# Optimization experiments

Hardware: AMD Instinct MI355X
Metric: run time of the kernel (lower is better)

The kernel has to match this reference:

```python
import jax, jax.numpy as jnp
import numpy as np

B = 4096        # number of (drug, disease) pair graphs
N_PER = 60      # nodes per subgraph (>= k)
N = B * N_PER   # 245760 total nodes
E = 2_000_000   # edges
F_IN = 64
L1, L2 = 32, 32 # latent_dim
K = 30          # sort-pool k
N_DRUG, N_DIS = 1024, 2048


def gcn_conv(x, src, dst, W, b, n):
    # PyG GCNConv (eval): h = XW; symmetric norm with self-loops; out = A_hat h + b
    h = x @ W
    deg = jax.ops.segment_sum(jnp.ones(src.shape[0], h.dtype), dst, num_segments=n) + 1.0
    dinv = deg ** -0.5
    msg = h[src] * (dinv[src] * dinv[dst])[:, None]
    out = jax.ops.segment_sum(msg, dst, num_segments=n)
    out = out + h * (dinv * dinv)[:, None]  # self-loop contribution
    return out + b


def dense_gcn(x, adj, W, b):
    # PyG DenseGCNConv: set diag to 1, D^-1/2 A D^-1/2, out = A_hat (x W) + b
    n = adj.shape[0]
    eye = jnp.eye(n, dtype=adj.dtype)
    a = adj * (1.0 - eye) + eye
    deg = a.sum(-1)
    dinv = jnp.where(deg > 0, deg ** -0.5, 0.0)
    a = dinv[:, None] * a * dinv[None, :]
    return a @ (x @ W) + b


def conv1d(x, w, b, stride):
    out = jax.lax.conv_general_dilated(x, w, (stride,), 'VALID',
                                       dimension_numbers=('NCH', 'OIH', 'NCH'))
    return out + b[None, :, None]


def setup_inputs():
    key = jax.random.key(0)
    ks = jax.random.split(key, 24)
    x = jax.random.normal(ks[0], (N, F_IN), jnp.float32)
    edge_index = jax.random.randint(ks[1], (2, E), 0, N)
    batch = jnp.repeat(jnp.arange(B), N_PER)
    node = jnp.stack([jax.random.randint(ks[2], (B,), 0, N_DRUG),
                      jax.random.randint(ks[3], (B,), 0, N_DIS)], axis=1)
    di_sim = jax.random.normal(ks[4], (N_DRUG, N_DRUG), jnp.float32)
    dr_sim = jax.random.normal(ks[5], (N_DIS, N_DIS), jnp.float32)
    drug_adj = jax.random.uniform(ks[6], (N_DRUG, N_DRUG), jnp.float32)
    dis_adj = jax.random.uniform(ks[7], (N_DIS, N_DIS), jnp.float32)
    p = jnp.array(0.5, jnp.float32)

    def w(k, shape):
        return jax.random.normal(k, shape, jnp.float32) * 0.05

    z = lambda s: jnp.zeros(s, jnp.float32)
    params = dict(
        W1=w(ks[8], (F_IN, L1)), b1=z((L1,)),
        W2=w(ks[9], (L1, L2)), b2=z((L2,)),
        W3=w(ks[10], (256, 64)), b3=z((64,)),
        W4=w(ks[11], (64, 16)), b4=z((16,)),
        lin_di_w=w(ks[12], (N_DRUG, 256)), lin_di_b=z((256,)),
        lin_dr_w=w(ks[13], (N_DIS, 256)), lin_dr_b=z((256,)),
        c1_w=w(ks[14], (128, 1, L1 + L2)), c1_b=z((128,)),
        c2_w=w(ks[15], (256, 128, 5)), c2_b=z((256,)),
        lin1_w=w(ks[16], (2816, 128)), lin1_b=z((128,)),
        lin2_w=w(ks[17], (128, 32)), lin2_b=z((32,)),
        bn_g=jnp.ones((32,), jnp.float32), bn_b=z((32,)),
        fcs_w=w(ks[18], (64, 32)), fcs_b=z((32,)),
        fcs2_w=w(ks[19], (32, 1)), fcs2_b=z((1,)),
    )
    return dict(x=x, edge_index=edge_index, batch=batch, node=node,
                di_sim=di_sim, dr_sim=dr_sim, drug_adj=drug_adj,
                dis_adj=dis_adj, p=p, **params)


def reference(x, edge_index, batch, node, di_sim, dr_sim, drug_adj, dis_adj, p,
              W1, b1, W2, b2, W3, b3, W4, b4,
              lin_di_w, lin_di_b, lin_dr_w, lin_dr_b,
              c1_w, c1_b, c2_w, c2_b, lin1_w, lin1_b, lin2_w, lin2_b,
              bn_g, bn_b, fcs_w, fcs_b, fcs2_w, fcs2_b):
    src, dst = edge_index[0], edge_index[1]
    # two GCN layers over the pair subgraphs
    x1 = jax.nn.relu(gcn_conv(x, src, dst, W1, b1, N))
    x2 = jax.nn.relu(gcn_conv(x1, src, dst, W2, b2, N))
    cs = jnp.concatenate([x1, x2], axis=1)       # [N, 64]
    D = cs.shape[1]
    # sort-pool: equal-size graphs, batch contiguous -> reshape and sort per graph
    xb = cs.reshape(B, N_PER, D)
    order = jnp.argsort(-xb[:, :, -1], axis=-1)  # descending by last channel
    xs = jnp.take_along_axis(xb, order[:, :, None], axis=1)[:, :K]  # [B, K, D]
    h = xs.reshape(B, 1, K * D)
    h = jax.nn.relu(conv1d(h, c1_w, c1_b, D))    # [B, 128, K]
    h = jax.lax.reduce_window(h, -jnp.inf, jax.lax.max, (1, 1, 2), (1, 1, 2), 'VALID')
    h = jax.nn.relu(conv1d(h, c2_w, c2_b, 1))    # [B, 256, 11]
    h = h.reshape(B, -1)                         # [B, 2816]
    h = jax.nn.relu(h @ lin1_w + lin1_b)
    h = h @ lin2_w + lin2_b
    h = jax.nn.relu(h * bn_g + bn_b)             # BatchNorm eval (mean 0, var 1)
    # dense similarity-graph branches (conv3/conv4 weights shared across branches)
    di_e = di_sim @ lin_di_w + lin_di_b
    di_f = jax.nn.relu(dense_gcn(di_e, drug_adj, W3, b3))
    di_o = jax.nn.relu(dense_gcn(di_f, drug_adj, W4, b4))
    di = di_o[node[:, 0]]
    dr_e = dr_sim @ lin_dr_w + lin_dr_b
    dr_f = jax.nn.relu(dense_gcn(dr_e, dis_adj, W3, b3))
    dr_o = jax.nn.relu(dense_gcn(dr_f, dis_adj, W4, b4))
    dr = dr_o[node[:, 1]]
    feat = jnp.concatenate([di, dr], axis=1)     # [B, 32]
    z = jnp.concatenate([h * p, feat * (1.0 - p)], axis=1)  # [B, 64]
    z = jax.nn.relu(z @ fcs_w + fcs_b)
    return (z @ fcs2_w + fcs2_b)[:, 0]
```

## Files before the change

kernel.cpp:

```cpp
#include <hip/hip_runtime.h>

#define NN 245760
#define NB 4096
#define NPER 60
#define NE 2000000
#define KSEL 30
#define NDRUG 1024
#define NDIS 2048
#define NBKT 480
#define CHUNK 8192
#define SEGCAP 4992

typedef unsigned short ushort_t;
typedef unsigned int uint_t;
using bf16x8 = __attribute__((ext_vector_type(8))) short;
using f32x4 = __attribute__((ext_vector_type(4))) float;

__device__ inline ushort_t f2bf(float f) {
    union { float f; unsigned int u; } v; v.f = f;
    unsigned int r = v.u + 0x7FFF + ((v.u >> 16) & 1);
    return (ushort_t)(r >> 16);
}

__global__ void k_bcount(const int* __restrict__ ei, int* __restrict__ bcnt) {
    __shared__ int h[NBKT];
    int t = threadIdx.x;
    for (int i = t; i < NBKT; i += 256) h[i] = 0;
    __syncthreads();
    for (int e = blockIdx.x * 256 + t; e < NE; e += gridDim.x * 256)
        atomicAdd(&h[ei[NE + e] >> 9], 1);
    __syncthreads();
    for (int i = t; i < NBKT; i += 256) if (h[i]) atomicAdd(&bcnt[i], h[i]);
}

__global__ void k_bscan(const int* __restrict__ bcnt, int* __restrict__ bofs) {
    __shared__ int a[512], b_[512];
    int t = threadIdx.x;
    int v = (t < NBKT) ? bcnt[t] : 0;
    a[t] = v; __syncthreads();
    int* src = a; int* dst = b_;
    for (int off = 1; off < 512; off <<= 1) {
        dst[t] = src[t] + ((t >= off) ? src[t - off] : 0);
        __syncthreads();
        int* tmp = src; src = dst; dst = tmp;
    }
    if (t < NBKT) bofs[t] = src[t] - v;
}

__global__ __launch_bounds__(256) void k_bscatter(const int* __restrict__ ei,
                                                  const int* __restrict__ bofs,
                                                  int* __restrict__ bfill,
                                                  uint_t* __restrict__ pairs) {
    __shared__ int hist[NBKT], fill[NBKT], gbase[NBKT];
    int t = threadIdx.x;
    long e0 = (long)blockIdx.x * CHUNK;
    int cnt = (int)min((long)CHUNK, (long)NE - e0);
    for (int i = t; i < NBKT; i += 256) { hist[i] = 0; fill[i] = 0; }
    __syncthreads();
    for (int i = t; i < cnt; i += 256)
        atomicAdd(&hist[ei[NE + e0 + i] >> 9], 1);
    __syncthreads();
    for (int i = t; i < NBKT; i += 256)
        if (hist[i]) gbase[i] = bofs[i] + atomicAdd(&bfill[i], hist[i]);
    __syncthreads();
    for (int i = t; i < cnt; i += 256) {
        int s = ei[e0 + i], d = ei[NE + e0 + i];
        int b = d >> 9;
        int pos = gbase[b] + atomicAdd(&fill[b], 1);
        pairs[pos] = ((uint_t)s << 9) | (uint_t)(d & 511);
    }
}

__global__ __launch_bounds__(256) void k_bbuild(const uint_t* __restrict__ pairs,
                                                const int* __restrict__ bofs,
                                                const int* __restrict__ bcnt,
                                                int* __restrict__ csr,
                                                int* __restrict__ rowp,
                                                int* __restrict__ cntg,
                                                float* __restrict__ dinv) {
    __shared__ int hist[512], nbase[512], nfill[512], scanA[512], scanB[512];
    __shared__ int seg[SEGCAP];
    int t = threadIdx.x, b = blockIdx.x;
    int ebase = bofs[b], ecnt = bcnt[b];
    if (ecnt > SEGCAP) ecnt = SEGCAP;
    for (int i = t; i < 512; i += 256) { hist[i] = 0; nfill[i] = 0; }
    __syncthreads();
    for (int i = t; i < ecnt; i += 256)
        atomicAdd(&hist[pairs[ebase + i] & 511], 1);
    __syncthreads();
    for (int i = t; i < 512; i += 256) scanA[i] = hist[i];
    __syncthreads();
    int* src = scanA; int* dst = scanB;
    for (int off = 1; off < 512; off <<= 1) {
        for (int i = t; i < 512; i += 256)
            dst[i] = src[i] + ((i >= off) ? src[i - off] : 0);
        __syncthreads();
        int* tmp = src; src = dst; dst = tmp;
    }
    for (int i = t; i < 512; i += 256) {
        int h = hist[i];
        int excl = src[i] - h;
        nbase[i] = excl;
        int n = (b << 9) + i;
        rowp[n] = ebase + excl;
        cntg[n] = h;
        dinv[n] = 1.0f / sqrtf((float)h + 1.0f);
    }
    __syncthreads();
    for (int i = t; i < ecnt; i += 256) {
        uint_t v = pairs[ebase + i];
        int ln = v & 511;
        int pos = nbase[ln] + atomicAdd(&nfill[ln], 1);
        if (pos < SEGCAP) seg[pos] = (int)(v >> 9);
    }
    __syncthreads();
    for (int i = t; i < ecnt; i += 256) csr[ebase + i] = seg[i];
}

__global__ __launch_bounds__(256) void k_xw(const float* __restrict__ A, const float* __restrict__ W,
                                            float* __restrict__ h, int K, int lda) {
    __shared__ float Xs[64][65];
    __shared__ float Ws[64][32];
    int t = threadIdx.x;
    int r0 = blockIdx.x * 64;
    int kq = K >> 2;
    for (int idx = t; idx < 64 * kq; idx += 256) {
        int row = idx / kq, q = idx % kq;
        float4 v = *(const float4*)(A + (long)(r0 + row) * lda + q * 4);
        Xs[row][q * 4 + 0] = v.x; Xs[row][q * 4 + 1] = v.y;
        Xs[row][q * 4 + 2] = v.z; Xs[row][q * 4 + 3] = v.w;
    }
    for (int idx = t; idx < K * 32; idx += 256) ((float*)Ws)[idx] = W[idx];
    __syncthreads();
    int r = (t >> 3) * 2, c = (t & 7) * 4;
    float4 acc0 = {0, 0, 0, 0}, acc1 = {0, 0, 0, 0};
    for (int k = 0; k < K; k++) {
        float x0 = Xs[r][k], x1 = Xs[r + 1][k];
        float4 w = *(const float4*)&Ws[k][c];
        acc0.x += x0 * w.x; acc0.y += x0 * w.y; acc0.z += x0 * w.z; acc0.w += x0 * w.w;
        acc1.x += x1 * w.x; acc1.y += x1 * w.y; acc1.z += x1 * w.z; acc1.w += x1 * w.w;
    }
    *(float4*)(h + (long)(r0 + r) * 32 + c) = acc0;
    *(float4*)(h + (long)(r0 + r + 1) * 32 + c) = acc1;
}

__global__ void k_gcn_agg(const float* __restrict__ h, const int* __restrict__ csr,
                          const int* __restrict__ rowp, const int* __restrict__ cnt,
                          const float* __restrict__ dinv, const float* __restrict__ bias,
                          float* __restrict__ out, int colofs) {
    int t = threadIdx.x;
    int l = t & 7, g = t >> 3;
    int d = blockIdx.x * 32 + g;
    float dd = dinv[d];
    int start = rowp[d], c = cnt[d];
    float4 hv = *(const float4*)(h + (long)d * 32 + l * 4);
    float4 acc; acc.x = dd * hv.x; acc.y = dd * hv.y; acc.z = dd * hv.z; acc.w = dd * hv.w;
    for (int k = 0; k < c; k++) {
        int s = csr[start + k];
        float ds = dinv[s];
        float4 v = *(const float4*)(h + (long)s * 32 + l * 4);
        acc.x += ds * v.x; acc.y += ds * v.y; acc.z += ds * v.z; acc.w += ds * v.w;
    }
    float4 bv = *(const float4*)(bias + l * 4);
    float* op = out + (long)d * 64 + colofs + l * 4;
    op[0] = fmaxf(dd * acc.x + bv.x, 0.f);
    op[1] = fmaxf(dd * acc.y + bv.y, 0.f);
    op[2] = fmaxf(dd * acc.z + bv.z, 0.f);
    op[3] = fmaxf(dd * acc.w + bv.w, 0.f);
}

__global__ __launch_bounds__(256, 2) void k_conv1_mfma(const float* __restrict__ cs,
                                                       const int* __restrict__ sel,
                                                       const ushort_t* __restrict__ c1w16,
                                                       const float* __restrict__ c1b,
                                                       ushort_t* __restrict__ po16) {
    __shared__ ushort_t A_lds[128 * 72];
    __shared__ ushort_t B_lds[128 * 72];
    int t = threadIdx.x;
    int r0 = blockIdx.x * 128;
#pragma unroll
    for (int rnd = 0; rnd < 4; rnd++) {
        int idx = t + rnd * 256;
        int row = idx >> 3, seg = idx & 7;
        const float* src = cs + (long)sel[r0 + row] * 64 + seg * 8;
        float4 v0 = *(const float4*)src;
        float4 v1 = *(const float4*)(src + 4);
        ushort_t tmp[8] = {f2bf(v0.x), f2bf(v0.y), f2bf(v0.z), f2bf(v0.w),
                           f2bf(v1.x), f2bf(v1.y), f2bf(v1.z), f2bf(v1.w)};
        *(uint4*)&A_lds[row * 72 + seg * 8] = *(uint4*)tmp;
        *(uint4*)&B_lds[row * 72 + seg * 8] = *(const uint4*)(c1w16 + row * 64 + seg * 8);
    }
    __syncthreads();
    int wv = t >> 6, lane = t & 63;
    int wm = wv >> 1, wn = wv & 1;
    int lrow = lane & 15, lk = (lane >> 4) * 8, lr4 = (lane >> 4) * 4;
    f32x4 acc[4][4] = {};
#pragma unroll
    for (int kk = 0; kk < 2; kk++) {
        bf16x8 a[4], b[4];
#pragma unroll
        for (int f = 0; f < 4; f++) {
            a[f] = *(const bf16x8*)&A_lds[(wm * 64 + f * 16 + lrow) * 72 + kk * 32 + lk];
            b[f] = *(const bf16x8*)&B_lds[(wn * 64 + f * 16 + lrow) * 72 + kk * 32 + lk];
        }
#pragma unroll
        for (int i = 0; i < 4; i++)
#pragma unroll
            for (int j = 0; j < 4; j++)
                acc[i][j] = __builtin_amdgcn_mfma_f32_16x16x32_bf16(a[i], b[j], acc[i][j], 0, 0, 0);
    }
    __syncthreads();
    ushort_t* po_lds = A_lds;
#pragma unroll
    for (int fn = 0; fn < 4; fn++) {
        int col = wn * 64 + fn * 16 + lrow;
        float bb = c1b[col];
#pragma unroll
        for (int fm = 0; fm < 4; fm++) {
            int lrow2 = wm * 32 + fm * 8 + (lr4 >> 1);
            float v0 = fmaxf(acc[fm][fn][0] + bb, 0.f);
            float v1 = fmaxf(acc[fm][fn][1] + bb, 0.f);
            float v2 = fmaxf(acc[fm][fn][2] + bb, 0.f);
            float v3 = fmaxf(acc[fm][fn][3] + bb, 0.f);
            po_lds[lrow2 * 128 + col]       = f2bf(fmaxf(v0, v1));
            po_lds[(lrow2 + 1) * 128 + col] = f2bf(fmaxf(v2, v3));
        }
    }
    __syncthreads();
    uint4* dst = (uint4*)(po16 + (long)(r0 >> 1) * 128);
    const uint4* srcp = (const uint4*)po_lds;
#pragma unroll
    for (int i = 0; i < 4; i++) dst[t + i * 256] = srcp[t + i * 256];
}

__global__ __launch_bounds__(256, 2) void k_conv2_mfma(const ushort_t* __restrict__ pool16,
                                                       const ushort_t* __restrict__ w2colT,
                                                       ushort_t* __restrict__ act2,
                                                       const float* __restrict__ bias) {
    __shared__ ushort_t smem[2 * 128 * 72];
    ushort_t* A_lds = smem;
    ushort_t* B_lds = smem + 128 * 72;
    int t = threadIdx.x;
    int r0 = blockIdx.x * 128, c0 = blockIdx.y * 128;
    long abase[4]; const ushort_t* bptr[4]; int lofs[4];
#pragma unroll
    for (int rnd = 0; rnd < 4; rnd++) {
        int idx = t + rnd * 256;
        int row = idx >> 3, seg = idx & 7;
        int arow = r0 + row;
        int bb = arow / 11, tt2 = arow - bb * 11;
        abase[rnd] = (long)(bb * 15 + tt2) * 128 + seg * 8;
        bptr[rnd] = w2colT + (long)(c0 + row) * 640 + seg * 8;
        lofs[rnd] = row * 72 + seg * 8;
    }
    int wv = t >> 6, lane = t & 63;
    int wm = wv >> 1, wn = wv & 1;
    int lrow = lane & 15, lk = (lane >> 4) * 8, lr4 = (lane >> 4) * 4;
    f32x4 acc[4][4] = {};
    for (int k0 = 0; k0 < 640; k0 += 64) {
#pragma unroll
        for (int rnd = 0; rnd < 4; rnd++) {
            *(uint4*)&A_lds[lofs[rnd]] = *(const uint4*)(pool16 + abase[rnd] + k0);
            *(uint4*)&B_lds[lofs[rnd]] = *(const uint4*)(bptr[rnd] + k0);
        }
        __syncthreads();
#pragma unroll
        for (int kk = 0; kk < 2; kk++) {
            bf16x8 a[4], b[4];
#pragma unroll
            for (int f = 0; f < 4; f++) {
                a[f] = *(const bf16x8*)&A_lds[(wm * 64 + f * 16 + lrow) * 72 + kk * 32 + lk];
                b[f] = *(const bf16x8*)&B_lds[(wn * 64 + f * 16 + lrow) * 72 + kk * 32 + lk];
            }
#pragma unroll
            for (int i = 0; i < 4; i++)
#pragma unroll
                for (int j = 0; j < 4; j++)
                    acc[i][j] = __builtin_amdgcn_mfma_f32_16x16x32_bf16(a[i], b[j], acc[i][j], 0, 0, 0);
        }
        __syncthreads();
    }
    ushort_t* c_lds = smem;
#pragma unroll
    for (int fn = 0; fn < 4; fn++) {
        int col = wn * 64 + fn * 16 + lrow;
        float bv = bias[c0 + col];
#pragma unroll
        for (int fm = 0; fm < 4; fm++) {
            int lr = wm * 64 + fm * 16 + lr4;
#pragma unroll
            for (int j = 0; j < 4; j++)
                c_lds[(lr + j) * 128 + col] = f2bf(fmaxf(acc[fm][fn][j] + bv, 0.f));
        }
    }
    __syncthreads();
#pragma unroll
    for (int i = 0; i < 8; i++) {
        int idx = t + i * 256;
        int row = idx >> 4, q = idx & 15;
        *(uint4*)(act2 + (long)(r0 + row) * 256 + c0 + q * 8) = ((const uint4*)c_lds)[idx];
    }
}

__global__ __launch_bounds__(256, 2) void k_lin1_mfma(const ushort_t* __restrict__ A,
                                                      const ushort_t* __restrict__ Bm,
                                                      float* __restrict__ C) {
    __shared__ ushort_t A_lds[128 * 72];
    __shared__ ushort_t B_lds[128 * 72];
    int t = threadIdx.x;
    int r0 = blockIdx.x * 128;
    int kz = blockIdx.z;
    const ushort_t* ap[4]; const ushort_t* bp[4]; int lofs[4];
#pragma unroll
    for (int rnd = 0; rnd < 4; rnd++) {
        int idx = t + rnd * 256;
        int row = idx >> 3, seg = idx & 7;
        ap[rnd] = A + (long)(r0 + row) * 2816 + kz * 704 + seg * 8;
        bp[rnd] = Bm + (long)row * 2816 + kz * 704 + seg * 8;
        lofs[rnd] = row * 72 + seg * 8;
    }
    int wv = t >> 6, lane = t & 63;
    int wm = wv >> 1, wn = wv & 1;
    int lrow = lane & 15, lk = (lane >> 4) * 8, lr4 = (lane >> 4) * 4;
    f32x4 acc[4][4] = {};
    for (int k0 = 0; k0 < 704; k0 += 64) {
#pragma unroll
        for (int rnd = 0; rnd < 4; rnd++) {
            *(uint4*)&A_lds[lofs[rnd]] = *(const uint4*)(ap[rnd] + k0);
            *(uint4*)&B_lds[lofs[rnd]] = *(const uint4*)(bp[rnd] + k0);
        }
        __syncthreads();
#pragma unroll
        for (int kk = 0; kk < 2; kk++) {
            bf16x8 a[4], b[4];
#pragma unroll
            for (int f = 0; f < 4; f++) {
                a[f] = *(const bf16x8*)&A_lds[(wm * 64 + f * 16 + lrow) * 72 + kk * 32 + lk];
                b[f] = *(const bf16x8*)&B_lds[(wn * 64 + f * 16 + lrow) * 72 + kk * 32 + lk];
            }
#pragma unroll
            for (int i = 0; i < 4; i++)
#pragma unroll
                for (int j = 0; j < 4; j++)
                    acc[i][j] = __builtin_amdgcn_mfma_f32_16x16x32_bf16(a[i], b[j], acc[i][j], 0, 0, 0);
        }
        __syncthreads();
    }
#pragma unroll
    for (int fn = 0; fn < 4; fn++) {
        int col = wn * 64 + fn * 16 + lrow;
#pragma unroll
        for (int fm = 0; fm < 4; fm++) {
            int rowb = r0 + wm * 64 + fm * 16 + lr4;
#pragma unroll
            for (int j = 0; j < 4; j++)
                atomicAdd(&C[(long)(rowb + j) * 128 + col], acc[fm][fn][j]);
        }
    }
}

__global__ __launch_bounds__(256, 2) void k_de_mfma(
    const ushort_t* __restrict__ A0, const ushort_t* __restrict__ B0, float* __restrict__ C0,
    const float* __restrict__ bias0, int M0, int K0, int KS0,
    const ushort_t* __restrict__ A1, const ushort_t* __restrict__ B1, float* __restrict__ C1,
    const float* __restrict__ bias1, int M1, int K1, int KS1) {
    __shared__ ushort_t A_lds[128 * 72];
    __shared__ ushort_t B_lds[64 * 72];
    int z = blockIdx.z;
    const ushort_t* A; const ushort_t* Bm; float* C; const float* bias; int M, K, kz, KS;
    if (z < KS0) { A = A0; Bm = B0; C = C0; bias = bias0; M = M0; K = K0; kz = z; KS = KS0; }
    else { A = A1; Bm = B1; C = C1; bias = bias1; M = M1; K = K1; kz = z - KS0; KS = KS1; }
    int r0 = blockIdx.x * 128, c0 = blockIdx.y * 64;
    if (r0 >= M) return;
    int Kc = K / KS;
    int kb = kz * Kc;
    int t = threadIdx.x;
    const ushort_t* ap[4]; int alofs[4];
#pragma unroll
    for (int rnd = 0; rnd < 4; rnd++) {
        int idx = t + rnd * 256;
        int row = idx >> 3, seg = idx & 7;
        ap[rnd] = A + (long)(r0 + row) * K + kb + seg * 8;
        alofs[rnd] = row * 72 + seg * 8;
    }
    const ushort_t* bp[2]; int blofs[2];
#pragma unroll
    for (int rnd = 0; rnd < 2; rnd++) {
        int idx = t + rnd * 256;
        int row = idx >> 3, seg = idx & 7;
        bp[rnd] = Bm + (long)(c0 + row) * K + kb + seg * 8;
        blofs[rnd] = row * 72 + seg * 8;
    }
    int wv = t >> 6, lane = t & 63;
    int lrow = lane & 15, lk = (lane >> 4) * 8, lr4 = (lane >> 4) * 4;
    uint4 areg[4], breg[2];
#pragma unroll
    for (int rnd = 0; rnd < 4; rnd++) areg[rnd] = *(const uint4*)(ap[rnd]);
#pragma unroll
    for (int rnd = 0; rnd < 2; rnd++) breg[rnd] = *(const uint4*)(bp[rnd]);
    f32x4 acc[2][4] = {};
    for (int k0 = 0; k0 < Kc; k0 += 64) {
#pragma unroll
        for (int rnd = 0; rnd < 4; rnd++) *(uint4*)&A_lds[alofs[rnd]] = areg[rnd];
#pragma unroll
        for (int rnd = 0; rnd < 2; rnd++) *(uint4*)&B_lds[blofs[rnd]] = breg[rnd];
        __syncthreads();
        if (k0 + 64 < Kc) {
#pragma unroll
            for (int rnd = 0; rnd < 4; rnd++) areg[rnd] = *(const uint4*)(ap[rnd] + k0 + 64);
#pragma unroll
            for (int rnd = 0; rnd < 2; rnd++) breg[rnd] = *(const uint4*)(bp[rnd] + k0 + 64);
        }
#pragma unroll
        for (int kk = 0; kk < 2; kk++) {
            bf16x8 a[2], b[4];
#pragma unroll
            for (int f = 0; f < 2; f++)
                a[f] = *(const bf16x8*)&A_lds[(wv * 32 + f * 16 + lrow) * 72 + kk * 32 + lk];
#pragma unroll
            for (int f = 0; f < 4; f++)
                b[f] = *(const bf16x8*)&B_lds[(f * 16 + lrow) * 72 + kk * 32 + lk];
#pragma unroll
            for (int i = 0; i < 2; i++)
#pragma unroll
                for (int j = 0; j < 4; j++)
                    acc[i][j] = __builtin_amdgcn_mfma_f32_16x16x32_bf16(a[i], b[j], acc[i][j], 0, 0, 0);
        }
        __syncthreads();
    }
#pragma unroll
    for (int fn = 0; fn < 4; fn++) {
        int col = c0 + fn * 16 + lrow;
        float bv = (kz == 0) ? bias[col] : 0.f;
#pragma unroll
        for (int fm = 0; fm < 2; fm++) {
            int rowb = r0 + wv * 32 + fm * 16 + lr4;
#pragma unroll
            for (int j = 0; j < 4; j++)
                atomicAdd(&C[(long)(rowb + j) * 256 + col], acc[fm][fn][j] + bv);
        }
    }
}

__global__ void k_cvt2(const float* __restrict__ a0, ushort_t* __restrict__ o0, long n0,
                       const float* __restrict__ a1, ushort_t* __restrict__ o1, long n1) {
    long i4 = ((long)blockIdx.x * 256 + threadIdx.x) * 4;
    const float* a; ushort_t* o;
    if (i4 < n0) { a = a0 + i4; o = o0 + i4; }
    else {
        long j = i4 - n0;
        if (j >= n1) return;
        a = a1 + j; o = o1 + j;
    }
    float4 v = *(const float4*)a;
    o[0] = f2bf(v.x); o[1] = f2bf(v.y); o[2] = f2bf(v.z); o[3] = f2bf(v.w);
}

__global__ void k_linwT2(const float* __restrict__ w0, ushort_t* __restrict__ o0, int K0,
                         const float* __restrict__ w1, ushort_t* __restrict__ o1, int K1) {
    __shared__ float tile[64][65];
    int nb0 = K0 / 64;
    int bx = blockIdx.x;
    const float* w; ushort_t* o; int K, kt;
    if (bx < nb0) { w = w0; o = o0; K = K0; kt = bx; }
    else { w = w1; o = o1; K = K1; kt = bx - nb0; }
    int n0 = blockIdx.y * 64, k0 = kt * 64;
    int t = threadIdx.x;
    int r = t >> 6, c = t & 63;
    for (int rr = r; rr < 64; rr += 4)
        tile[rr][c] = w[(long)(k0 + rr) * 256 + n0 + c];
    __syncthreads();
    for (int rr = r; rr < 64; rr += 4)
        o[(long)(n0 + rr) * K + k0 + c] = f2bf(tile[c][rr]);
}

__global__ __launch_bounds__(256) void k_gemm_sk(
    const float* A0, const float* B0, float* C0, const float* ab0p, const float* cs0p,
    int M0, int N0, int K0, int lda0, int KS0, int Kc0,
    const float* A1, const float* B1, float* C1, const float* ab1p, const float* cs1p,
    int M1, int N1, int K1, int lda1, int KS1, int Kc1) {
    int z = blockIdx.z;
    const float* A; const float* Bm; float* C; const float* abp; const float* csp;
    int M, N, K, lda, kz, Kc;
    if (z < KS0) { A = A0; Bm = B0; C = C0; abp = ab0p; csp = cs0p; M = M0; N = N0; K = K0; lda = lda0; kz = z; Kc = Kc0; }
    else { A = A1; Bm = B1; C = C1; abp = ab1p; csp = cs1p; M = M1; N = N1; K = K1; lda = lda1; kz = z - KS0; Kc = Kc1; }
    int r0 = blockIdx.x * 64, c0 = blockIdx.y * 64;
    if (r0 >= M || c0 >= N) return;
    int kb = kz * Kc, ke = min(K, kb + Kc);
    __shared__ float As[16][68];
    __shared__ float Bs[16][68];
    int t = threadIdx.x;
    int tx = t & 15, ty = t >> 4;
    float acc[4][4] = {};
    int ar = t >> 2, aq = (t & 3) * 4;
    long abase = (long)(r0 + ar) * lda;
    int brow = t >> 4, bc = (t & 15) * 4;
    for (int k0 = kb; k0 < ke; k0 += 16) {
        float4 av = *(const float4*)(A + abase + k0 + aq);
        if (abp) {
            float4 abv = *(const float4*)(abp + k0 + aq);
            av.x += abv.x; av.y += abv.y; av.z += abv.z; av.w += abv.w;
        }
        As[aq + 0][ar] = av.x; As[aq + 1][ar] = av.y; As[aq + 2][ar] = av.z; As[aq + 3][ar] = av.w;
        float4 bv = *(const float4*)(Bm + (long)(k0 + brow) * N + c0 + bc);
        *(float4*)&Bs[brow][bc] = bv;
        __syncthreads();
#pragma unroll
        for (int kk = 0; kk < 16; kk++) {
            float4 a4 = *(const float4*)&As[kk][ty * 4];
            float4 b4 = *(const float4*)&Bs[kk][tx * 4];
            float aa[4] = {a4.x, a4.y, a4.z, a4.w};
            float bb2[4] = {b4.x, b4.y, b4.z, b4.w};
#pragma unroll
            for (int i = 0; i < 4; i++)
#pragma unroll
                for (int j = 0; j < 4; j++) acc[i][j] += aa[i] * bb2[j];
        }
        __syncthreads();
    }
#pragma unroll
    for (int i = 0; i < 4; i++) {
        int row = r0 + ty * 4 + i;
        float sc = csp ? csp[row] : 1.0f;
#pragma unroll
        for (int j = 0; j < 4; j++)
            atomicAdd(&C[(long)row * N + c0 + tx * 4 + j], acc[i][j] * sc);
    }
}

__global__ void k_dense_deg2(const float* __restrict__ adj0, float* __restrict__ d0, int n0,
                             const float* __restrict__ adj1, float* __restrict__ d1, int n1) {
    int lane = threadIdx.x & 63;
    int row = (blockIdx.x * blockDim.x + threadIdx.x) >> 6;
    const float* adj; float* dv; int n, r;
    if (row < n0) { adj = adj0; dv = d0; n = n0; r = row; }
    else {
        r = row - n0;
        if (r >= n1) return;
        adj = adj1; dv = d1; n = n1;
    }
    const float* rp = adj + (long)r * n;
    float s = 0.f;
    for (int j = lane; j < n; j += 64) s += rp[j];
    for (int off = 32; off > 0; off >>= 1) s += __shfl_down(s, off, 64);
    if (lane == 0) {
        float deg = s - rp[r] + 1.0f;
        dv[r] = (deg > 0.f) ? 1.0f / sqrtf(deg) : 0.f;
    }
}

__global__ void k_fix_w4(const float* g0, const float* u0, const float* adj0, const float* d0, float* o0, int n0,
                         const float* g1, const float* u1, const float* adj1, const float* d1, float* o1, int n1,
                         const float* __restrict__ b3, const float* __restrict__ W4) {
    __shared__ float dfs[16][68];
    __shared__ float W4s[64 * 16];
    int t = threadIdx.x;
    for (int i = t; i < 1024; i += 256) W4s[i] = W4[i];
    int bx = blockIdx.x, nb0 = n0 / 16;
    const float* g; const float* u; const float* adj; const float* dv; float* o; int n, r0;
    if (bx < nb0) { g = g0; u = u0; adj = adj0; dv = d0; o = o0; n = n0; r0 = bx * 16; }
    else { g = g1; u = u1; adj = adj1; dv = d1; o = o1; n = n1; r0 = (bx - nb0) * 16; }
    int r = t >> 4;
    int row = r0 + r;
    float di = dv[row];
    float om = 1.0f - adj[(long)row * n + row];
    int c4 = (t & 15) * 4;
    float4 gv = *(const float4*)(g + (long)row * 64 + c4);
    float4 uv = *(const float4*)(u + (long)row * 64 + c4);
    float4 bv = *(const float4*)(b3 + c4);
    dfs[r][c4 + 0] = fmaxf(di * (gv.x + om * uv.x) + bv.x, 0.f);
    dfs[r][c4 + 1] = fmaxf(di * (gv.y + om * uv.y) + bv.y, 0.f);
    dfs[r][c4 + 2] = fmaxf(di * (gv.z + om * uv.z) + bv.z, 0.f);
    dfs[r][c4 + 3] = fmaxf(di * (gv.w + om * uv.w) + bv.w, 0.f);
    __syncthreads();
    int c = t & 15;
    float accv = 0.f;
#pragma unroll
    for (int k = 0; k < 64; k++) accv += dfs[r][k] * W4s[k * 16 + c];
    o[row * 16 + c] = di * accv;
}

__global__ void k_fixup2(const float* g0, const float* t0, const float* adj0, const float* d0, float* C0, long n0,
                         const float* g1, const float* t1, const float* adj1, const float* d1, float* C1, long n1,
                         const float* bias, int cols) {
    long idx = (long)blockIdx.x * 256 + threadIdx.x;
    long s0 = n0 * cols;
    const float* g; const float* tt; const float* adj; const float* dv; float* C; long n, li;
    if (idx < s0) { g = g0; tt = t0; adj = adj0; dv = d0; C = C0; n = n0; li = idx; }
    else {
        li = idx - s0;
        if (li >= n1 * cols) return;
        g = g1; tt = t1; adj = adj1; dv = d1; C = C1; n = n1;
    }
    long i = li / cols; int j = li % cols;
    float v = dv[i] * (g[li] + (1.0f - adj[i * n + i]) * tt[li]) + bias[j];
    C[li] = fmaxf(v, 0.f);
}

__global__ void k_adj16(const float* adj0, const float* u0, float* C0, int n0, int KS0, int Kc0,
                        const float* adj1, const float* u1, float* C1, int n1, int KS1, int Kc1) {
    int z = blockIdx.z;
    const float* adj; const float* u; float* C; int n, kz, Kc;
    if (z < KS0) { adj = adj0; u = u0; C = C0; n = n0; kz = z; Kc = Kc0; }
    else { adj = adj1; u = u1; C = C1; n = n1; kz = z - KS0; Kc = Kc1; }
    int r0 = blockIdx.x * 16;
    if (r0 >= n) return;
    int t = threadIdx.x;
    int r = r0 + (t >> 4), c = t & 15;
    int kb = kz * Kc, ke = min(n, kb + Kc);
    const float* arp = adj + (long)r * n;
    float acc = 0.f;
    for (int k = kb; k < ke; k += 4) {
        float4 a = *(const float4*)(arp + k);
        acc += a.x * u[(k + 0) * 16 + c] + a.y * u[(k + 1) * 16 + c]
             + a.z * u[(k + 2) * 16 + c] + a.w * u[(k + 3) * 16 + c];
    }
    atomicAdd(&C[r * 16 + c], acc);
}

__global__ void k_select(const float* __restrict__ cs, int* __restrict__ sel) {
    __shared__ float kk[240];
    int t = threadIdx.x;
    int b0 = blockIdx.x * 4;
    if (t < 240) kk[t] = cs[((long)(b0 * 60 + t)) * 64 + 63];
    __syncthreads();
    if (t < 240) {
        int lb = t / 60, i = t % 60;
        float key = kk[lb * 60 + i];
        int r = 0;
        for (int j = 0; j < 60; j++) {
            float kj = kk[lb * 60 + j];
            r += (kj > key) || (kj == key && j < i);
        }
        if (r < KSEL) sel[(b0 + lb) * KSEL + r] = (b0 + lb) * 60 + i;
    }
}

__global__ void k_w2colT(const float* __restrict__ c2w, ushort_t* __restrict__ o) {
    int idx = blockIdx.x * blockDim.x + threadIdx.x;
    if (idx >= 256 * 640) return;
    int oc = idx / 640, q = idx % 640;
    int tap = q >> 7, ic = q & 127;
    o[idx] = f2bf(c2w[(oc * 128 + ic) * 5 + tap]);
}

__global__ void k_w1pT(const float* __restrict__ w, ushort_t* __restrict__ o) {
    int idx = blockIdx.x * blockDim.x + threadIdx.x;
    if (idx >= 128 * 2816) return;
    int j = idx / 2816, c = idx % 2816;
    int tt = c >> 8, oc = c & 255;
    o[idx] = f2bf(w[(oc * 11 + tt) * 128 + j]);
}

__global__ void k_lin2_bn(const float* __restrict__ x, const float* __restrict__ l1b,
                          const float* __restrict__ w,
                          const float* __restrict__ b, const float* __restrict__ g,
                          const float* __restrict__ bb, float* __restrict__ o) {
    int t = blockIdx.x * blockDim.x + threadIdx.x;
    int j = t & 31, bi = t >> 5;
    const float* xr = x + (long)bi * 128;
    float acc = b[j];
    for (int k = 0; k < 128; k++) acc += fmaxf(xr[k] + l1b[k], 0.f) * w[k * 32 + j];
    o[bi * 32 + j] = fmaxf(acc * g[j] + bb[j], 0.f);
}

__global__ __launch_bounds__(256) void k_final(const float* __restrict__ hfin, const int* __restrict__ node,
                                               const float* __restrict__ dio, const float* __restrict__ dro,
                                               const float* __restrict__ pp,
                                               const float* __restrict__ fw, const float* __restrict__ fb,
                                               const float* __restrict__ f2w, const float* __restrict__ f2b,
                                               float* __restrict__ out) {
    __shared__ float w[64 * 32];
    __shared__ float w2[32];
    int t = threadIdx.x;
    for (int f = t; f < 2048; f += 256) w[f] = fw[f];
    if (t < 32) w2[t] = f2w[t];
    __syncthreads();
    int b = blockIdx.x * 256 + t;
    float p = *pp, q = 1.0f - p;
    float zin[64];
#pragma unroll
    for (int i = 0; i < 32; i++) zin[i] = hfin[b * 32 + i] * p;
    int n0 = node[b * 2], n1 = node[b * 2 + 1];
#pragma unroll
    for (int i = 0; i < 16; i++) zin[32 + i] = dio[n0 * 16 + i] * q;
#pragma unroll
    for (int i = 0; i < 16; i++) zin[48 + i] = dro[n1 * 16 + i] * q;
    float res = f2b[0];
    for (int j = 0; j < 32; j++) {
        float acc = fb[j];
#pragma unroll
        for (int i = 0; i < 64; i++) acc += zin[i] * w[i * 32 + j];
        res += fmaxf(acc, 0.f) * w2[j];
    }
    out[b] = res;
}

extern "C" void kernel_launch(void* const* d_in, const int* in_sizes, int n_in,
                              void* d_out, int out_size, void* d_ws, size_t ws_size,
                              hipStream_t stream) {
    const float* x        = (const float*)d_in[0];
    const int*   ei       = (const int*)d_in[1];
    const int*   node     = (const int*)d_in[3];
    const float* di_sim   = (const float*)d_in[4];
    const float* dr_sim   = (const float*)d_in[5];
    const float* drug_adj = (const float*)d_in[6];
    const float* dis_adj  = (const float*)d_in[7];
    const float* p        = (const float*)d_in[8];
    const float* W1 = (const float*)d_in[9],  *b1 = (const float*)d_in[10];
    const float* W2 = (const float*)d_in[11], *b2 = (const float*)d_in[12];
    const float* W3 = (const float*)d_in[13], *b3 = (const float*)d_in[14];
    const float* W4 = (const float*)d_in[15], *b4 = (const float*)d_in[16];
    const float* lin_di_w = (const float*)d_in[17], *lin_di_b = (const float*)d_in[18];
    const float* lin_dr_w = (const float*)d_in[19], *lin_dr_b = (const float*)d_in[20];
    const float* c1w = (const float*)d_in[21], *c1b = (const float*)d_in[22];
    const float* c2w = (const float*)d_in[23], *c2b = (const float*)d_in[24];
    const float* lin1w = (const float*)d_in[25], *lin1b = (const float*)d_in[26];
    const float* lin2w = (const float*)d_in[27], *lin2b = (const float*)d_in[28];
    const float* bng = (const float*)d_in[29], *bnb = (const float*)d_in[30];
    const float* fcsw = (const float*)d_in[31], *fcsb = (const float*)d_in[32];
    const float* fcs2w = (const float*)d_in[33], *fcs2b = (const float*)d_in[34];

    char* ws = (char*)d_ws;
    size_t o = 0;
    auto alloc = [&](size_t bytes) { size_t r = o; o += (bytes + 255) & ~(size_t)255; return r; };
    int*   csr     = (int*)(ws + alloc((size_t)NE * 4));
    int*   rowp    = (int*)(ws + alloc((size_t)NN * 4));
    int*   degcnt  = (int*)(ws + alloc((size_t)NN * 4));
    float* dinvn   = (float*)(ws + alloc((size_t)NN * 4));
    float* hbuf    = (float*)(ws + alloc((size_t)NN * 32 * 4));
    float* cs      = (float*)(ws + alloc((size_t)NN * 64 * 4));
    int*   sel     = (int*)(ws + alloc((size_t)NB * KSEL * 4));
    float* hfin    = (float*)(ws + alloc((size_t)NB * 32 * 4));
    ushort_t* w2colT = (ushort_t*)(ws + alloc((size_t)256 * 640 * 2));
    ushort_t* w1pT   = (ushort_t*)(ws + alloc((size_t)128 * 2816 * 2));
    int*   bofs    = (int*)(ws + alloc((size_t)NBKT * 4));
    float* ddin_di = (float*)(ws + alloc((size_t)NDRUG * 4));
    float* ddin_dr = (float*)(ws + alloc((size_t)NDIS * 4));
    float* dt2_di  = (float*)(ws + alloc((size_t)NDRUG * 16 * 4));
    float* dt2_dr  = (float*)(ws + alloc((size_t)NDIS * 16 * 4));
    float* do_di   = (float*)(ws + alloc((size_t)NDRUG * 16 * 4));
    float* do_dr   = (float*)(ws + alloc((size_t)NDIS * 16 * 4));
    size_t zbase = o;
    int*   bcnt    = (int*)(ws + alloc((size_t)NBKT * 4));
    int*   bfill   = (int*)(ws + alloc((size_t)NBKT * 4));
    float* lin1o   = (float*)(ws + alloc((size_t)NB * 128 * 4));
    float* de_di   = (float*)(ws + alloc((size_t)NDRUG * 256 * 4));
    float* de_dr   = (float*)(ws + alloc((size_t)NDIS * 256 * 4));
    float* dt_di   = (float*)(ws + alloc((size_t)NDRUG * 64 * 4));
    float* dt_dr   = (float*)(ws + alloc((size_t)NDIS * 64 * 4));
    float* dg_di   = (float*)(ws + alloc((size_t)NDRUG * 64 * 4));
    float* dg_dr   = (float*)(ws + alloc((size_t)NDIS * 64 * 4));
    float* dg2_di  = (float*)(ws + alloc((size_t)NDRUG * 16 * 4));
    float* dg2_dr  = (float*)(ws + alloc((size_t)NDIS * 16 * 4));
    size_t zsize = o - zbase;
    uint_t* pairsg   = (uint_t*)cs;
    ushort_t* pool16 = (ushort_t*)hbuf;
    ushort_t* act2   = (ushort_t*)cs;
    char* hb = (char*)hbuf;
    ushort_t* di_sim16 = (ushort_t*)(hb + 15728640);
    ushort_t* dr_sim16 = (ushort_t*)(hb + 17825792);
    ushort_t* lindiT16 = (ushort_t*)(hb + 26214400);
    ushort_t* lindrT16 = (ushort_t*)(hb + 26738688);
    ushort_t* c1w16    = (ushort_t*)(hb + 27787264);

    hipMemsetAsync(ws + zbase, 0, zsize, stream);

    k_bcount<<<512, 256, 0, stream>>>(ei, bcnt);
    k_bscan<<<1, 512, 0, stream>>>(bcnt, bofs);
    k_bscatter<<<(NE + CHUNK - 1) / CHUNK, 256, 0, stream>>>(ei, bofs, bfill, pairsg);
    k_bbuild<<<NBKT, 256, 0, stream>>>(pairsg, bofs, bcnt, csr, rowp, degcnt, dinvn);

    k_xw<<<NN / 64, 256, 0, stream>>>(x, W1, hbuf, 64, 64);
    k_gcn_agg<<<NN / 32, 256, 0, stream>>>(hbuf, csr, rowp, degcnt, dinvn, b1, cs, 0);
    k_xw<<<NN / 64, 256, 0, stream>>>(cs, W2, hbuf, 32, 64);
    k_gcn_agg<<<NN / 32, 256, 0, stream>>>(hbuf, csr, rowp, degcnt, dinvn, b2, cs, 32);

    k_select<<<NB / 4, 256, 0, stream>>>(cs, sel);

    k_cvt2<<<5120, 256, 0, stream>>>(di_sim, di_sim16, (long)NDRUG * NDRUG,
                                     dr_sim, dr_sim16, (long)NDIS * NDIS);
    k_linwT2<<<dim3(48, 4), 256, 0, stream>>>(lin_di_w, lindiT16, NDRUG,
                                              lin_dr_w, lindrT16, NDIS);
    k_de_mfma<<<dim3(16, 4, 12), 256, 0, stream>>>(
        di_sim16, lindiT16, de_di, lin_di_b, NDRUG, NDRUG, 4,
        dr_sim16, lindrT16, de_dr, lin_dr_b, NDIS, NDIS, 8);
    k_dense_deg2<<<(NDRUG + NDIS) * 64 / 256, 256, 0, stream>>>(drug_adj, ddin_di, NDRUG, dis_adj, ddin_dr, NDIS);

    k_cvt2<<<8, 256, 0, stream>>>(c1w, c1w16, 8192, c1w, c1w16, 0);
    k_w2colT<<<(256 * 640 + 255) / 256, 256, 0, stream>>>(c2w, w2colT);
    k_w1pT<<<(128 * 2816 + 255) / 256, 256, 0, stream>>>(lin1w, w1pT);

    k_conv1_mfma<<<960, 256, 0, stream>>>(cs, sel, c1w16, c1b, pool16);

    k_conv2_mfma<<<dim3(352, 2), 256, 0, stream>>>(pool16, w2colT, act2, c2b);

    k_lin1_mfma<<<dim3(32, 1, 4), 256, 0, stream>>>(act2, w1pT, lin1o);
    k_lin2_bn<<<NB * 32 / 256, 256, 0, stream>>>(lin1o, lin1b, lin2w, lin2b, bng, bnb, hfin);

    k_gemm_sk<<<dim3(NDIS / 64, 1, 8), 256, 0, stream>>>(
        de_di, W3, dt_di, nullptr, ddin_di, NDRUG, 64, 256, 256, 4, 64,
        de_dr, W3, dt_dr, nullptr, ddin_dr, NDIS, 64, 256, 256, 4, 64);
    k_gemm_sk<<<dim3(NDIS / 64, 1, 24), 256, 0, stream>>>(
        drug_adj, dt_di, dg_di, nullptr, nullptr, NDRUG, 64, NDRUG, NDRUG, 8, 128,
        dis_adj, dt_dr, dg_dr, nullptr, nullptr, NDIS, 64, NDIS, NDIS, 16, 128);
    k_fix_w4<<<(NDRUG + NDIS) / 16, 256, 0, stream>>>(
        dg_di, dt_di, drug_adj, ddin_di, dt2_di, NDRUG,
        dg_dr, dt_dr, dis_adj, ddin_dr, dt2_dr, NDIS, b3, W4);
    k_adj16<<<dim3(NDIS / 16, 1, 6), 256, 0, stream>>>(
        drug_adj, dt2_di, dg2_di, NDRUG, 2, 512,
        dis_adj, dt2_dr, dg2_dr, NDIS, 4, 512);
    k_fixup2<<<((NDRUG + NDIS) * 16 + 255) / 256, 256, 0, stream>>>(
        dg2_di, dt2_di, drug_adj, ddin_di, do_di, NDRUG,
        dg2_dr, dt2_dr, dis_adj, ddin_dr, do_dr, NDIS, b4, 16);

    k_final<<<NB / 256, 256, 0, stream>>>(hfin, node, do_di, do_dr, p, fcsw, fcsb, fcs2w, fcs2b, (float*)d_out);
}
```

Baseline: 499.3 us.

## Aggregate GCN messages per destination bucket with LDS atomics instead of CSR

Drops the per-node CSR build and replaces it with a small kernel that only computes degree inverses from the destination-bucketed pairs. Each GCN aggregation block now takes one 512-node destination bucket, sorts its edges in LDS by source block for gather locality, and accumulates messages into a padded LDS accumulator with float atomics. The self-loop, bias and ReLU are applied when the accumulator is written out. This removes the CSR write and read traffic, but each block needs roughly 95KB of LDS across only 480 blocks. That limits occupancy and latency hiding for the random gathers, and adds LDS atomic contention.

```diff
diff --git a/kernel.cpp b/kernel.cpp
--- a/kernel.cpp
+++ b/kernel.cpp
@@ -71,50 +71,20 @@
     }
 }
 
-__global__ __launch_bounds__(256) void k_bbuild(const uint_t* __restrict__ pairs,
-                                                const int* __restrict__ bofs,
-                                                const int* __restrict__ bcnt,
-                                                int* __restrict__ csr,
-                                                int* __restrict__ rowp,
-                                                int* __restrict__ cntg,
-                                                float* __restrict__ dinv) {
-    __shared__ int hist[512], nbase[512], nfill[512], scanA[512], scanB[512];
-    __shared__ int seg[SEGCAP];
+__global__ __launch_bounds__(256) void k_bdeg(const uint_t* __restrict__ pairs,
+                                              const int* __restrict__ bofs,
+                                              const int* __restrict__ bcnt,
+                                              float* __restrict__ dinv) {
+    __shared__ int hist[512];
     int t = threadIdx.x, b = blockIdx.x;
-    int ebase = bofs[b], ecnt = bcnt[b];
-    if (ecnt > SEGCAP) ecnt = SEGCAP;
-    for (int i = t; i < 512; i += 256) { hist[i] = 0; nfill[i] = 0; }
+    int ebase = bofs[b], ecnt = min(bcnt[b], SEGCAP);
+    for (int i = t; i < 512; i += 256) hist[i] = 0;
     __syncthreads();
     for (int i = t; i < ecnt; i += 256)
         atomicAdd(&hist[pairs[ebase + i] & 511], 1);
     __syncthreads();
-    for (int i = t; i < 512; i += 256) scanA[i] = hist[i];
-    __syncthreads();
-    int* src = scanA; int* dst = scanB;
-    for (int off = 1; off < 512; off <<= 1) {
-        for (int i = t; i < 512; i += 256)
-            dst[i] = src[i] + ((i >= off) ? src[i - off] : 0);
-        __syncthreads();
-        int* tmp = src; src = dst; dst = tmp;
-    }
-    for (int i = t; i < 512; i += 256) {
-        int h = hist[i];
-        int excl = src[i] - h;
-        nbase[i] = excl;
-        int n = (b << 9) + i;
-        rowp[n] = ebase + excl;
-        cntg[n] = h;
-        dinv[n] = 1.0f / sqrtf((float)h + 1.0f);
-    }
-    __syncthreads();
-    for (int i = t; i < ecnt; i += 256) {
-        uint_t v = pairs[ebase + i];
-        int ln = v & 511;
-        int pos = nbase[ln] + atomicAdd(&nfill[ln], 1);
-        if (pos < SEGCAP) seg[pos] = (int)(v >> 9);
-    }
-    __syncthreads();
-    for (int i = t; i < ecnt; i += 256) csr[ebase + i] = seg[i];
+    for (int i = t; i < 512; i += 256)
+        dinv[(b << 9) + i] = 1.0f / sqrtf((float)hist[i] + 1.0f);
 }
 
 __global__ __launch_bounds__(256) void k_xw(const float* __restrict__ A, const float* __restrict__ W,
@@ -144,29 +114,83 @@
     *(float4*)(h + (long)(r0 + r + 1) * 32 + c) = acc1;
 }
 
-__global__ void k_gcn_agg(const float* __restrict__ h, const int* __restrict__ csr,
-                          const int* __restrict__ rowp, const int* __restrict__ cnt,
-                          const float* __restrict__ dinv, const float* __restrict__ bias,
-                          float* __restrict__ out, int colofs) {
-    int t = threadIdx.x;
+__global__ __launch_bounds__(256) void k_gcn_agg2(const float* __restrict__ h,
+                                                  const uint_t* __restrict__ pairs,
+                                                  const int* __restrict__ bofs,
+                                                  const int* __restrict__ bcnt,
+                                                  const float* __restrict__ dinv,
+                                                  const float* __restrict__ bias,
+                                                  float* __restrict__ out, int colofs) {
+    __shared__ float accl[512 * 33];
+    __shared__ uint_t ps[SEGCAP];
+    __shared__ int hist[512], scanA[512], scanB[512], ofs[512];
+    int t = threadIdx.x, b = blockIdx.x;
+    int ebase = bofs[b], ecnt = min(bcnt[b], SEGCAP);
+    for (int i = t; i < 512 * 33; i += 256) accl[i] = 0.f;
+    for (int i = t; i < 512; i += 256) hist[i] = 0;
+    __syncthreads();
+    for (int i = t; i < ecnt; i += 256)
+        atomicAdd(&hist[pairs[ebase + i] >> 18], 1);
+    __syncthreads();
+    for (int i = t; i < 512; i += 256) scanA[i] = hist[i];
+    __syncthreads();
+    int* src = scanA; int* dst = scanB;
+    for (int off = 1; off < 512; off <<= 1) {
+        for (int i = t; i < 512; i += 256)
+            dst[i] = src[i] + ((i >= off) ? src[i - off] : 0);
+        __syncthreads();
+        int* tmp = src; src = dst; dst = tmp;
+    }
+    for (int i = t; i < 512; i += 256) ofs[i] = src[i] - hist[i];
+    __syncthreads();
+    for (int i = t; i < ecnt; i += 256) {
+        uint_t v = pairs[ebase + i];
+        int pos = atomicAdd(&ofs[v >> 18], 1);
+        ps[pos] = v;
+    }
+    __syncthreads();
     int l = t & 7, g = t >> 3;
-    int d = blockIdx.x * 32 + g;
-    float dd = dinv[d];
-    int start = rowp[d], c = cnt[d];
-    float4 hv = *(const float4*)(h + (long)d * 32 + l * 4);
-    float4 acc; acc.x = dd * hv.x; acc.y = dd * hv.y; acc.z = dd * hv.z; acc.w = dd * hv.w;
-    for (int k = 0; k < c; k++) {
-        int s = csr[start + k];
-        float ds = dinv[s];
-        float4 v = *(const float4*)(h + (long)s * 32 + l * 4);
-        acc.x += ds * v.x; acc.y += ds * v.y; acc.z += ds * v.z; acc.w += ds * v.w;
-    }
-    float4 bv = *(const float4*)(bias + l * 4);
-    float* op = out + (long)d * 64 + colofs + l * 4;
-    op[0] = fmaxf(dd * acc.x + bv.x, 0.f);
-    op[1] = fmaxf(dd * acc.y + bv.y, 0.f);
-    op[2] = fmaxf(dd * acc.z + bv.z, 0.f);
-    op[3] = fmaxf(dd * acc.w + bv.w, 0.f);
+    for (int e = g; e < ecnt; e += 64) {
+        uint_t v0 = ps[e];
+        int s0 = v0 >> 9, d0 = v0 & 511;
+        float ds0 = dinv[s0];
+        float4 h0 = *(const float4*)(h + (long)s0 * 32 + l * 4);
+        int e1 = e + 32;
+        uint_t v1 = 0; float4 h1; float ds1 = 0.f; int d1 = 0;
+        if (e1 < ecnt) {
+            v1 = ps[e1];
+            int s1 = v1 >> 9; d1 = v1 & 511;
+            ds1 = dinv[s1];
+            h1 = *(const float4*)(h + (long)s1 * 32 + l * 4);
+        }
+        float* a0 = &accl[d0 * 33 + l * 4];
+        atomicAdd(&a0[0], ds0 * h0.x);
+        atomicAdd(&a0[1], ds0 * h0.y);
+        atomicAdd(&a0[2], ds0 * h0.z);
+        atomicAdd(&a0[3], ds0 * h0.w);
+        if (e1 < ecnt) {
+            float* a1 = &accl[d1 * 33 + l * 4];
+            atomicAdd(&a1[0], ds1 * h1.x);
+            atomicAdd(&a1[1], ds1 * h1.y);
+            atomicAdd(&a1[2], ds1 * h1.z);
+            atomicAdd(&a1[3], ds1 * h1.w);
+        }
+    }
+    __syncthreads();
+    for (int i = t; i < 4096; i += 256) {
+        int ld = i >> 3, ll = i & 7;
+        int d = (b << 9) + ld;
+        float dd = dinv[d];
+        float4 hv = *(const float4*)(h + (long)d * 32 + ll * 4);
+        float4 bv = *(const float4*)(bias + ll * 4);
+        float* ap = &accl[ld * 33 + ll * 4];
+        float4 ov;
+        ov.x = fmaxf(dd * (ap[0] + dd * hv.x) + bv.x, 0.f);
+        ov.y = fmaxf(dd * (ap[1] + dd * hv.y) + bv.y, 0.f);
+        ov.z = fmaxf(dd * (ap[2] + dd * hv.z) + bv.z, 0.f);
+        ov.w = fmaxf(dd * (ap[3] + dd * hv.w) + bv.w, 0.f);
+        *(float4*)(out + (long)d * 64 + colofs + ll * 4) = ov;
+    }
 }
 
 __global__ __launch_bounds__(256, 2) void k_conv1_mfma(const float* __restrict__ cs,
@@ -724,9 +748,7 @@
     char* ws = (char*)d_ws;
     size_t o = 0;
     auto alloc = [&](size_t bytes) { size_t r = o; o += (bytes + 255) & ~(size_t)255; return r; };
-    int*   csr     = (int*)(ws + alloc((size_t)NE * 4));
-    int*   rowp    = (int*)(ws + alloc((size_t)NN * 4));
-    int*   degcnt  = (int*)(ws + alloc((size_t)NN * 4));
+    uint_t* pairs_g = (uint_t*)(ws + alloc((size_t)NE * 4));
     float* dinvn   = (float*)(ws + alloc((size_t)NN * 4));
     float* hbuf    = (float*)(ws + alloc((size_t)NN * 32 * 4));
     float* cs      = (float*)(ws + alloc((size_t)NN * 64 * 4));
@@ -754,7 +776,6 @@
     float* dg2_di  = (float*)(ws + alloc((size_t)NDRUG * 16 * 4));
     float* dg2_dr  = (float*)(ws + alloc((size_t)NDIS * 16 * 4));
     size_t zsize = o - zbase;
-    uint_t* pairsg   = (uint_t*)cs;
     ushort_t* pool16 = (ushort_t*)hbuf;
     ushort_t* act2   = (ushort_t*)cs;
     char* hb = (char*)hbuf;
@@ -768,13 +789,13 @@
 
     k_bcount<<<512, 256, 0, stream>>>(ei, bcnt);
     k_bscan<<<1, 512, 0, stream>>>(bcnt, bofs);
-    k_bscatter<<<(NE + CHUNK - 1) / CHUNK, 256, 0, stream>>>(ei, bofs, bfill, pairsg);
-    k_bbuild<<<NBKT, 256, 0, stream>>>(pairsg, bofs, bcnt, csr, rowp, degcnt, dinvn);
+    k_bscatter<<<(NE + CHUNK - 1) / CHUNK, 256, 0, stream>>>(ei, bofs, bfill, pairs_g);
+    k_bdeg<<<NBKT, 256, 0, stream>>>(pairs_g, bofs, bcnt, dinvn);
 
     k_xw<<<NN / 64, 256, 0, stream>>>(x, W1, hbuf, 64, 64);
-    k_gcn_agg<<<NN / 32, 256, 0, stream>>>(hbuf, csr, rowp, degcnt, dinvn, b1, cs, 0);
+    k_gcn_agg2<<<NBKT, 256, 0, stream>>>(hbuf, pairs_g, bofs, bcnt, dinvn, b1, cs, 0);
     k_xw<<<NN / 64, 256, 0, stream>>>(cs, W2, hbuf, 32, 64);
-    k_gcn_agg<<<NN / 32, 256, 0, stream>>>(hbuf, csr, rowp, degcnt, dinvn, b2, cs, 32);
+    k_gcn_agg2<<<NBKT, 256, 0, stream>>>(hbuf, pairs_g, bofs, bcnt, dinvn, b2, cs, 32);
 
     k_select<<<NB / 4, 256, 0, stream>>>(cs, sel);
 
```

Measured after the change: 1.146 ms. 2.29x slower.
